# Performance work log

Hardware: AMD Instinct MI355X
Metric: run time of the kernel (lower is better)

## Reference

```python
import jax, jax.numpy as jnp
import numpy as np

D_MODEL, D_K, D_V, H = 1024, 128, 128, 8


def setup_inputs() -> dict:
    key = jax.random.key(0)
    ks = jax.random.split(key, 14)
    B, NQ, NK = 8, 1024, 1024
    def lin(kw, out_d, in_d):
        # xavier_uniform weight, zero bias
        lim = jnp.sqrt(6.0 / (in_d + out_d))
        return jax.random.uniform(kw, (out_d, in_d), jnp.float32, -lim, lim)
    return {
        "queries": jax.random.normal(ks[0], (B, NQ, D_MODEL), jnp.float32),
        "keys": jax.random.normal(ks[1], (B, NK, D_MODEL), jnp.float32),
        "values": jax.random.normal(ks[2], (B, NK, D_MODEL), jnp.float32),
        "language_signals": jax.random.normal(ks[3], (B, NQ, D_MODEL), jnp.float32),
        "Wq": lin(ks[4], H * D_K, D_MODEL), "bq": jnp.zeros((H * D_K,), jnp.float32),
        "Wk": lin(ks[5], H * D_K, D_MODEL), "bk": jnp.zeros((H * D_K,), jnp.float32),
        "Wv": lin(ks[6], H * D_V, D_MODEL), "bv": jnp.zeros((H * D_V,), jnp.float32),
        "Ws": lin(ks[7], H * D_K, D_MODEL), "bs": jnp.zeros((H * D_K,), jnp.float32),
        "Wo": lin(ks[8], D_MODEL, H * D_V), "bo": jnp.zeros((D_MODEL,), jnp.float32),
    }


def reference(queries, keys, values, language_signals,
              Wq, bq, Wk, bk, Wv, bv, Ws, bs, Wo, bo):
    b, nq, _ = queries.shape
    nk = keys.shape[1]
    scale = 1.0 / jnp.sqrt(jnp.asarray(D_K, queries.dtype))
    # project and split heads -> (b, h, n, d)
    q = (queries @ Wq.T + bq).reshape(b, nq, H, D_K).transpose(0, 2, 1, 3)
    s = (language_signals @ Ws.T + bs).reshape(b, nq, H, D_K).transpose(0, 2, 1, 3)
    k = (keys @ Wk.T + bk).reshape(b, nk, H, D_K).transpose(0, 2, 1, 3)
    v = (values @ Wv.T + bv).reshape(b, nk, H, D_V).transpose(0, 2, 1, 3)
    attn = jnp.einsum('bhqd,bhkd->bhqk', q, k) * scale           # (b,h,nq,nk)
    lang = jnp.einsum('bhqd,bhqd->bhq', q, s) * scale            # diagonal sentinel score
    combined = jnp.concatenate([attn, lang[..., None]], axis=-1)  # (b,h,nq,nk+1)
    p = jax.nn.softmax(combined, axis=-1)
    # per-query value set is [v; s_i]: split matmul into kv part + sentinel part
    out = jnp.einsum('bhqk,bhkd->bhqd', p[..., :nk], v) + p[..., nk:] * s
    out = out.transpose(0, 2, 1, 3).reshape(b, nq, H * D_V)
    return out @ Wo.T + bo
```

## Files before the change

### kernel.cpp

```cpp
#include <hip/hip_runtime.h>
#include <hip/hip_bf16.h>


typedef __attribute__((ext_vector_type(8))) short s16x8;
typedef __attribute__((ext_vector_type(4))) float f32x4;
typedef __attribute__((ext_vector_type(16))) float f32x16;
typedef __attribute__((ext_vector_type(4))) unsigned int u32x4;

#define DEVI static __device__ __forceinline__

constexpr int BATCH = 8;
constexpr int SEQ   = 1024;
constexpr int NH    = 8;
constexpr int DH    = 128;
constexpr int DM    = 1024;

DEVI short bf16r(float f) {
  __hip_bfloat16 h = __float2bfloat16(f);
  return *reinterpret_cast<short*>(&h);
}
DEVI float bf2f(short s) {
  __hip_bfloat16 h;
  *reinterpret_cast<short*>(&h) = s;
  return __bfloat162float(h);
}
DEVI s16x8 cvt8(const float4& a, const float4& b) {
  s16x8 r;
  r[0] = bf16r(a.x); r[1] = bf16r(a.y); r[2] = bf16r(a.z); r[3] = bf16r(a.w);
  r[4] = bf16r(b.x); r[5] = bf16r(b.y); r[6] = bf16r(b.z); r[7] = bf16r(b.w);
  return r;
}
DEVI unsigned int pack2bf(float a, float b) {
  return (unsigned int)(unsigned short)bf16r(a) |
         ((unsigned int)(unsigned short)bf16r(b) << 16);
}

#define GLOAD16(g, l)                                                        \
  __builtin_amdgcn_global_load_lds(                                          \
      (const __attribute__((address_space(1))) unsigned int*)(g),            \
      (__attribute__((address_space(3))) unsigned int*)(l), 16, 0, 0)

DEVI f32x4 mfma(s16x8 a, s16x8 b, f32x4 c) {
  return __builtin_amdgcn_mfma_f32_16x16x32_bf16(a, b, c, 0, 0, 0);
}
DEVI f32x16 mfma32(s16x8 a, s16x8 b, f32x16 c) {
  return __builtin_amdgcn_mfma_f32_32x32x16_bf16(a, b, c, 0, 0, 0);
}

__global__ __launch_bounds__(256)
void cvt_all(const float* __restrict__ a0, const float* __restrict__ a1,
             const float* __restrict__ a2, const float* __restrict__ a3,
             const float* __restrict__ w0, const float* __restrict__ w1,
             const float* __restrict__ w2, const float* __restrict__ w3,
             const float* __restrict__ w4,
             short* __restrict__ d0, short* __restrict__ d1,
             short* __restrict__ d2, short* __restrict__ d3,
             short* __restrict__ e0, short* __restrict__ e1,
             short* __restrict__ e2, short* __restrict__ e3,
             short* __restrict__ e4) {
  const float* s; short* d; int idx;
  int bid = blockIdx.x;
  if (bid < 16384) {
    int which = bid >> 12; idx = bid & 4095;
    switch (which) {
      case 0: s = a0; d = d0; break;
      case 1: s = a1; d = d1; break;
      case 2: s = a2; d = d2; break;
      default: s = a3; d = d3; break;
    }
  } else {
    int r = bid - 16384;
    int which = r >> 9; idx = r & 511;
    switch (which) {
      case 0: s = w0; d = e0; break;
      case 1: s = w1; d = e1; break;
      case 2: s = w2; d = e2; break;
      case 3: s = w3; d = e3; break;
      default: s = w4; d = e4; break;
    }
  }
  size_t i = ((size_t)idx * 256 + threadIdx.x) * 8;
  float4 a = *(const float4*)(s + i);
  float4 b = *(const float4*)(s + i + 4);
  *(s16x8*)(d + i) = cvt8(a, b);
}

DEVI void gemm_core(const short* __restrict__ A, const short* __restrict__ W,
                    short* Alds, short* Blds, int m0, int n0,
                    f32x4 (&acc)[4][4]) {
  const int tid = threadIdx.x, lane = tid & 63, wid = tid >> 6;
  const int wm = wid >> 1, wn = wid & 1, lr = lane & 15, lg = lane >> 4;
  const int srow = wid * 32 + (lane >> 3);
  const int scb  = (lane & 7) * 16;

  for (int k0 = 0; k0 < DM; k0 += 64) {
    if (k0) __syncthreads();
#pragma unroll
    for (int t = 0; t < 4; t++) {
      int row = srow + t * 8;
      int cbs = scb ^ ((row & 7) << 4);
      GLOAD16((const char*)A + ((size_t)(m0 + row) * DM + k0) * 2 + cbs,
              (char*)Alds + wid * 4096 + t * 1024);
      GLOAD16((const char*)W + ((size_t)(n0 + row) * DM + k0) * 2 + cbs,
              (char*)Blds + wid * 4096 + t * 1024);
    }
    __syncthreads();
#pragma unroll
    for (int kk = 0; kk < 2; kk++) {
      s16x8 af[4], bf[4];
#pragma unroll
      for (int i = 0; i < 4; i++) {
        int row = wm * 64 + i * 16 + lr;
        af[i] = *(const s16x8*)((const char*)Alds + row * 128 +
                                ((kk * 64 + lg * 16) ^ ((row & 7) << 4)));
      }
#pragma unroll
      for (int j = 0; j < 4; j++) {
        int row = wn * 64 + j * 16 + lr;
        bf[j] = *(const s16x8*)((const char*)Blds + row * 128 +
                                ((kk * 64 + lg * 16) ^ ((row & 7) << 4)));
      }
#pragma unroll
      for (int i = 0; i < 4; i++)
#pragma unroll
        for (int j = 0; j < 4; j++)
          acc[i][j] = mfma(af[i], bf[j], acc[i][j]);
    }
  }
}

__global__ __launch_bounds__(512, 2)
void proj_gemm256(const short* __restrict__ qa, const short* __restrict__ ka,
                  const short* __restrict__ va, const short* __restrict__ sa,
                  const short* __restrict__ wq, const short* __restrict__ wk,
                  const short* __restrict__ wv, const short* __restrict__ wsn,
                  const float* __restrict__ bq, const float* __restrict__ bk,
                  const float* __restrict__ bv, const float* __restrict__ bsn,
                  short* __restrict__ Qo, short* __restrict__ Ko,
                  short* __restrict__ Vo, short* __restrict__ So) {
  __shared__ short Alds[2][256 * 64];
  __shared__ short Blds[2][256 * 64];

  const int tid = threadIdx.x, lane = tid & 63, wid = tid >> 6;
  const int wm = wid >> 2, wn = wid & 3, lr = lane & 15, lg = lane >> 4;

  const int xcd = blockIdx.x & 7;
  const int r   = blockIdx.x >> 3;
  const int z   = xcd >> 1;
  const int m0  = (((xcd & 1) << 4) + (r >> 2)) << 8;
  const int n0  = (r & 3) << 8;

  const short* A; const short* W; const float* bias; short* C;
  switch (z) {
    case 0: A = qa; W = wq;  bias = bq;  C = Qo; break;
    case 1: A = ka; W = wk;  bias = bk;  C = Ko; break;
    case 2: A = va; W = wv;  bias = bv;  C = Vo; break;
    default: A = sa; W = wsn; bias = bsn; C = So; break;
  }
  const char* Ag = (const char*)A + (size_t)m0 * 2048;
  const char* Wg = (const char*)W + (size_t)n0 * 2048;

  const int sR  = wid * 8 + (lane >> 3);
  const int sCB = (((lane & 7) ^ (lane >> 3)) << 4);
  const int lgb = lg * 16, rsw = (lr & 7) << 4;
  const int ko0 = lgb ^ rsw, ko1 = (64 + lgb) ^ rsw;

#define STG(Gb, r0, kb, Lb, off)                                             \
  GLOAD16((Gb) + (size_t)((r0) + sR) * 2048 + (kb) + sCB,                    \
          (char*)(Lb) + (off) + wid * 1024)

  {
    char* pa0 = (char*)Alds[0]; char* pb0 = (char*)Blds[0];
    char* pa1 = (char*)Alds[1]; char* pb1 = (char*)Blds[1];
    STG(Ag,   0, 0, pa0, 0);     STG(Ag, 128, 0, pa0, 16384);
    STG(Ag,  64, 0, pa0, 8192);  STG(Ag, 192, 0, pa0, 24576);
    STG(Wg,   0, 0, pb0, 0);     STG(Wg,  64, 0, pb0, 8192);
    STG(Wg, 128, 0, pb0, 16384); STG(Wg, 192, 0, pb0, 24576);
    STG(Ag,   0, 128, pa1, 0);     STG(Ag, 128, 128, pa1, 16384);
    STG(Wg,   0, 128, pb1, 0);     STG(Wg,  64, 128, pb1, 8192);
    STG(Ag,  64, 128, pa1, 8192);  STG(Ag, 192, 128, pa1, 24576);
  }
  asm volatile("s_waitcnt vmcnt(6)" ::: "memory");
  __builtin_amdgcn_s_barrier();

  f32x4 acc[8][4] = {};
  const int rA0 = wm * 128 + lr;
  const int rB0 = wn * 64 + lr;

#pragma unroll 2
  for (int kt = 0; kt < 16; ++kt) {
    const char* Ab = (const char*)Alds[kt & 1];
    const char* Bb = (const char*)Blds[kt & 1];
    char* AbS = (char*)Alds[kt & 1];
    char* BbS = (char*)Blds[kt & 1];
    char* BbN = (char*)Blds[(kt + 1) & 1];
    const int kb1 = (kt + 1) * 128, kb2 = (kt + 2) * 128;

    s16x8 af[8], b0f[4], b1f[4];
#pragma unroll
    for (int mf = 0; mf < 4; mf++) {
      int ro = (rA0 + mf * 16) * 128;
      af[2 * mf]     = *(const s16x8*)(Ab + ro + ko0);
      af[2 * mf + 1] = *(const s16x8*)(Ab + ro + ko1);
    }
#pragma unroll
    for (int nf = 0; nf < 2; nf++) {
      int ro = (rB0 + nf * 16) * 128;
      b0f[2 * nf]     = *(const s16x8*)(Bb + ro + ko0);
      b0f[2 * nf + 1] = *(const s16x8*)(Bb + ro + ko1);
    }
    if (kt + 1 < 16) {
      STG(Wg, 128, kb1, BbN, 16384);
      STG(Wg, 192, kb1, BbN, 24576);
    }
    asm volatile("s_waitcnt lgkmcnt(8)" ::: "memory");
    __builtin_amdgcn_s_barrier();
    asm volatile("s_waitcnt lgkmcnt(0)" ::: "memory");
    __builtin_amdgcn_s_setprio(1);
#pragma unroll
    for (int mf = 0; mf < 4; mf++)
#pragma unroll
      for (int nf = 0; nf < 2; nf++) {
        acc[mf][nf] = mfma(af[2 * mf],     b0f[2 * nf],     acc[mf][nf]);
        acc[mf][nf] = mfma(af[2 * mf + 1], b0f[2 * nf + 1], acc[mf][nf]);
      }
    __builtin_amdgcn_s_setprio(0);
    __builtin_amdgcn_s_barrier();

#pragma unroll
    for (int nf = 0; nf < 2; nf++) {
      int ro = (rB0 + 32 + nf * 16) * 128;
      b1f[2 * nf]     = *(const s16x8*)(Bb + ro + ko0);
      b1f[2 * nf + 1] = *(const s16x8*)(Bb + ro + ko1);
    }
    if (kt + 2 < 16) {
      STG(Ag,   0, kb2, AbS, 0);
      STG(Ag, 128, kb2, AbS, 16384);
    }
    __builtin_amdgcn_s_barrier();
    asm volatile("s_waitcnt lgkmcnt(0)" ::: "memory");
    __builtin_amdgcn_s_setprio(1);
#pragma unroll
    for (int mf = 0; mf < 4; mf++)
#pragma unroll
      for (int nf = 0; nf < 2; nf++) {
        acc[mf][nf + 2] = mfma(af[2 * mf],     b1f[2 * nf],     acc[mf][nf + 2]);
        acc[mf][nf + 2] = mfma(af[2 * mf + 1], b1f[2 * nf + 1], acc[mf][nf + 2]);
      }
    __builtin_amdgcn_s_setprio(0);
    __builtin_amdgcn_s_barrier();

#pragma unroll
    for (int mf = 0; mf < 4; mf++) {
      int ro = (rA0 + 64 + mf * 16) * 128;
      af[2 * mf]     = *(const s16x8*)(Ab + ro + ko0);
      af[2 * mf + 1] = *(const s16x8*)(Ab + ro + ko1);
    }
    if (kt + 2 < 16) {
      STG(Wg,  0, kb2, BbS, 0);
      STG(Wg, 64, kb2, BbS, 8192);
    }
    __builtin_amdgcn_s_barrier();
    asm volatile("s_waitcnt lgkmcnt(0)" ::: "memory");
    __builtin_amdgcn_s_setprio(1);
#pragma unroll
    for (int mf = 0; mf < 4; mf++)
#pragma unroll
      for (int nf = 0; nf < 2; nf++) {
        acc[mf + 4][nf + 2] = mfma(af[2 * mf],     b1f[2 * nf],     acc[mf + 4][nf + 2]);
        acc[mf + 4][nf + 2] = mfma(af[2 * mf + 1], b1f[2 * nf + 1], acc[mf + 4][nf + 2]);
      }
    __builtin_amdgcn_s_setprio(0);
    __builtin_amdgcn_s_barrier();

    if (kt + 2 < 16) {
      STG(Ag,  64, kb2, AbS, 8192);
      STG(Ag, 192, kb2, AbS, 24576);
    }
    __builtin_amdgcn_s_barrier();
    __builtin_amdgcn_s_setprio(1);
#pragma unroll
    for (int mf = 0; mf < 4; mf++)
#pragma unroll
      for (int nf = 0; nf < 2; nf++) {
        acc[mf + 4][nf] = mfma(af[2 * mf],     b0f[2 * nf],     acc[mf + 4][nf]);
        acc[mf + 4][nf] = mfma(af[2 * mf + 1], b0f[2 * nf + 1], acc[mf + 4][nf]);
      }
    __builtin_amdgcn_s_setprio(0);
    if (kt < 14) asm volatile("s_waitcnt vmcnt(6)" ::: "memory");
    else         asm volatile("s_waitcnt vmcnt(0)" ::: "memory");
    __builtin_amdgcn_s_barrier();
  }
#undef STG

#pragma unroll
  for (int mf = 0; mf < 8; mf++) {
#pragma unroll
    for (int r2 = 0; r2 < 4; r2++) {
      int m = m0 + wm * 128 + mf * 16 + lg * 4 + r2;
      int bb = m >> 10, sq = m & 1023;
#pragma unroll
      for (int nf = 0; nf < 4; nf++) {
        int n = n0 + wn * 64 + nf * 16 + lr;
        float v = acc[mf][nf][r2] + bias[n];
        int hh = n >> 7, d = n & 127;
        if (z == 2)
          C[((size_t)(bb * NH + hh) * DH + d) * SEQ + sq] = bf16r(v);
        else
          C[((size_t)(bb * NH + hh) * SEQ + sq) * DH + d] = bf16r(v);
      }
    }
  }
}

__global__ __launch_bounds__(256)
void out_gemm(const short* __restrict__ A, const short* __restrict__ W,
              const float* __restrict__ bias, float* __restrict__ C) {
  __shared__ short Alds[128 * 64];
  __shared__ short Blds[128 * 64];
  const int bid = blockIdx.x;
  const int wg = (bid & 7) * 64 + (bid >> 3);
  const int m0 = (wg >> 3) * 128, n0 = (wg & 7) * 128;
  f32x4 acc[4][4] = {};
  gemm_core(A, W, Alds, Blds, m0, n0, acc);

  const int lane = threadIdx.x & 63, wid = threadIdx.x >> 6;
  const int wm = wid >> 1, wn = wid & 1, lr = lane & 15, lg = lane >> 4;
#pragma unroll
  for (int i = 0; i < 4; i++)
#pragma unroll
    for (int r = 0; r < 4; r++) {
      int m = m0 + wm * 64 + i * 16 + lg * 4 + r;
#pragma unroll
      for (int j = 0; j < 4; j++) {
        int n = n0 + wn * 64 + j * 16 + lr;
        C[(size_t)m * DM + n] = acc[i][j][r] + bias[n];
      }
    }
}

DEVI void stage_kv(const char* Kg, const char* Vg, int k0n,
                   short* Kd, short* Vd, int tid, int wave) {
  const int krow_l = tid >> 4, kslot = tid & 15;
  const int vrow_l = tid >> 3, vslot = tid & 7;
#pragma unroll
  for (int ln = 0; ln < 2; ln++) {
    int kr = ln * 32 + krow_l;
    int ss = kslot ^ (((kr & 7) << 1) ^ ((kr >> 3) & 3));
    GLOAD16(Kg + (size_t)(k0n + kr) * 256 + ss * 16,
            (char*)Kd + ln * 8192 + wave * 1024);
  }
#pragma unroll
  for (int ln = 0; ln < 2; ln++) {
    int dr = ln * 64 + vrow_l;
    int ss = vslot ^ ((dr & 7) ^ ((dr >> 3) & 3));
    GLOAD16(Vg + (size_t)dr * 2048 + (size_t)k0n * 2 + ss * 16,
            (char*)Vd + ln * 8192 + wave * 1024);
  }
}

__global__ __launch_bounds__(512, 2)
void attn_kernel(const short* __restrict__ Qb, const short* __restrict__ Kb,
                 const short* __restrict__ Vtb, const short* __restrict__ Sb,
                 short* __restrict__ att) {
  __shared__ short Klds[2][64 * 128];
  __shared__ short Vtlds[2][128 * 64];

  const int tid = threadIdx.x, lane = tid & 63, wave = tid >> 6;
  const int l31 = lane & 31, hi = lane >> 5;
  const int bid = blockIdx.x;
  const int logical = (bid & 7) * 32 + (bid >> 3);
  const int hb = logical >> 2, qt = logical & 3;
  const int b = hb >> 3, h = hb & 7;
  const int q0 = qt * 256 + wave * 32;
  const size_t base = (size_t)(b * NH + h) * SEQ * DH;
  const char* Kg = (const char*)(Kb + base);
  const char* Vg = (const char*)(Vtb + base);
  const float scale = 0.08838834764831845f * 1.44269504088896340f;

  s16x8 qf[8];
  {
    const char* qrow = (const char*)(Qb + base) + (size_t)(q0 + l31) * 256 + hi * 16;
#pragma unroll
    for (int kd = 0; kd < 8; kd++) qf[kd] = *(const s16x8*)(qrow + kd * 32);
  }

  float m_run = -INFINITY, l_run = 0.f;
  f32x16 oacc[4] = {};

  const int v4r = ((((lane & 7) << 1) ^ ((lane >> 3) & 3))) << 4;
  const int v3r = (((lane & 7) ^ ((lane >> 3) & 3))) << 4;

  stage_kv(Kg, Vg, 0, Klds[0], Vtlds[0], tid, wave);

  for (int it = 0; it < 16; ++it) {
    const int cur = it & 1;
    __syncthreads();
    if (it < 15)
      stage_kv(Kg, Vg, (it + 1) * 64, Klds[cur ^ 1], Vtlds[cur ^ 1], tid, wave);

    f32x16 st0 = {}, st1 = {};
    const char* Kb0 = (const char*)Klds[cur] + l31 * 256;
    __builtin_amdgcn_s_setprio(1);
#pragma unroll
    for (int kd = 0; kd < 8; kd++) {
      int co = (kd * 32 + hi * 16) ^ v4r;
      s16x8 a0 = *(const s16x8*)(Kb0 + co);
      s16x8 a1 = *(const s16x8*)(Kb0 + 32 * 256 + co);
      st0 = mfma32(a0, qf[kd], st0);
      st1 = mfma32(a1, qf[kd], st1);
    }
    __builtin_amdgcn_s_setprio(0);

    float traw = -INFINITY;
#pragma unroll
    for (int r = 0; r < 16; r++) {
      traw = fmaxf(traw, st0[r]);
      traw = fmaxf(traw, st1[r]);
    }
    traw = fmaxf(traw, __shfl_xor(traw, 32));
    float tmax = traw * scale;
    const bool skip = __all(tmax - m_run <= 8.f);
    float m_new = skip ? m_run : fmaxf(m_run, tmax);
    float psum = 0.f;
    unsigned W0[8], W1[8];
#pragma unroll
    for (int i = 0; i < 8; i++) {
      float p0 = exp2f(fmaf(st0[2 * i],     scale, -m_new));
      float p1 = exp2f(fmaf(st0[2 * i + 1], scale, -m_new));
      float p2 = exp2f(fmaf(st1[2 * i],     scale, -m_new));
      float p3 = exp2f(fmaf(st1[2 * i + 1], scale, -m_new));
      psum += (p0 + p1) + (p2 + p3);
      W0[i] = pack2bf(p0, p1);
      W1[i] = pack2bf(p2, p3);
    }
    psum += __shfl_xor(psum, 32);
    if (skip) {
      l_run += psum;
    } else {
      float fac = exp2f(m_run - m_new);
      l_run = l_run * fac + psum;
      m_run = m_new;
#pragma unroll
      for (int reg = 0; reg < 16; reg++) {
        int qs = (reg & 3) + 8 * (reg >> 2);
        float fr = __shfl(fac, qs + 4 * hi);
#pragma unroll
        for (int dt = 0; dt < 4; dt++) oacc[dt][reg] *= fr;
      }
    }

    s16x8 pa[4];
#pragma unroll
    for (int ks = 0; ks < 4; ks++) {
      const int s4 = (ks & 1) * 4;
      unsigned a0, a1, b0, b1;
      if (ks >> 1) { a0 = W1[s4]; a1 = W1[s4 + 1]; b0 = W1[s4 + 2]; b1 = W1[s4 + 3]; }
      else         { a0 = W0[s4]; a1 = W0[s4 + 1]; b0 = W0[s4 + 2]; b1 = W0[s4 + 3]; }
      unsigned snd0 = hi ? a0 : b0, snd1 = hi ? a1 : b1;
      unsigned rem0 = __shfl_xor(snd0, 32), rem1 = __shfl_xor(snd1, 32);
      unsigned w0 = hi ? rem0 : a0;
      unsigned w1 = hi ? rem1 : a1;
      unsigned w2 = hi ? b0 : rem0;
      unsigned w3 = hi ? b1 : rem1;
      u32x4 t4 = {w0, w1, w2, w3};
      pa[ks] = __builtin_bit_cast(s16x8, t4);
    }

    const char* Vb0 = (const char*)Vtlds[cur] + l31 * 128;
    __builtin_amdgcn_s_setprio(1);
#pragma unroll
    for (int dt = 0; dt < 4; dt++) {
#pragma unroll
      for (int ks = 0; ks < 4; ks++) {
        int co = (ks * 32 + hi * 16) ^ v3r;
        s16x8 bv = *(const s16x8*)(Vb0 + dt * 4096 + co);
        oacc[dt] = mfma32(pa[ks], bv, oacc[dt]);
      }
    }
    __builtin_amdgcn_s_setprio(0);
  }

  s16x8 sf[8];
  {
    const char* srow = (const char*)(Sb + base) + (size_t)(q0 + l31) * 256 + hi * 16;
#pragma unroll
    for (int kd = 0; kd < 8; kd++) sf[kd] = *(const s16x8*)(srow + kd * 32);
  }
  float dot = 0.f;
#pragma unroll
  for (int kd = 0; kd < 8; kd++)
#pragma unroll
    for (int j = 0; j < 8; j++) dot += bf2f(qf[kd][j]) * bf2f(sf[kd][j]);
  dot += __shfl_xor(dot, 32);
  float sc = dot * scale;
  float m_new = fmaxf(m_run, sc);
  float fac = exp2f(m_run - m_new);
  float ps = exp2f(sc - m_new);
  l_run = l_run * fac + ps;
  float inv_l = 1.f / l_run;

#pragma unroll
  for (int reg = 0; reg < 16; reg++) {
    int qs = (reg & 3) + 8 * (reg >> 2) + 4 * hi;
    int qsl = (reg & 3) + 8 * (reg >> 2);
    float fr = __shfl(fac,   qsl + 4 * hi);
    float pr = __shfl(ps,    qsl + 4 * hi);
    float il = __shfl(inv_l, qsl + 4 * hi);
    int qg = q0 + qs;
    const short* Sr = Sb + base + (size_t)qg * DH;
    short* orow = att + ((size_t)b * SEQ + qg) * (NH * DH) + h * DH;
#pragma unroll
    for (int dt = 0; dt < 4; dt++) {
      int d = dt * 32 + l31;
      float v = oacc[dt][reg] * fr + pr * bf2f(Sr[d]);
      orow[d] = bf16r(v * il);
    }
  }
}

extern "C" void kernel_launch(void* const* d_in, const int* in_sizes, int n_in,
                              void* d_out, int out_size, void* d_ws, size_t ws_size,
                              hipStream_t stream) {
  const float* queries = (const float*)d_in[0];
  const float* keys    = (const float*)d_in[1];
  const float* values  = (const float*)d_in[2];
  const float* lang    = (const float*)d_in[3];
  const float* Wq = (const float*)d_in[4];  const float* bq = (const float*)d_in[5];
  const float* Wk = (const float*)d_in[6];  const float* bk = (const float*)d_in[7];
  const float* Wv = (const float*)d_in[8];  const float* bv = (const float*)d_in[9];
  const float* Ws = (const float*)d_in[10]; const float* bs = (const float*)d_in[11];
  const float* Wo = (const float*)d_in[12]; const float* bo = (const float*)d_in[13];
  float* out = (float*)d_out;

  short* ws = (short*)d_ws;
  const size_t NE = (size_t)BATCH * SEQ * DM;
  const size_t WE = (size_t)DM * DM;
  short* qbf = ws;
  short* kbf = qbf + NE;
  short* vbf = kbf + NE;
  short* sbf = vbf + NE;
  short* Qb  = sbf + NE;
  short* Kb  = Qb  + NE;
  short* Vtb = Kb  + NE;
  short* Sb  = Vtb + NE;
  short* wqb = Sb  + NE;
  short* wkb = wqb + WE;
  short* wvb = wkb + WE;
  short* wsb = wvb + WE;
  short* wob = wsb + WE;
  short* att = qbf;

  hipLaunchKernelGGL(cvt_all, dim3(16384 + 2560), dim3(256), 0, stream,
                     queries, keys, values, lang, Wq, Wk, Wv, Ws, Wo,
                     qbf, kbf, vbf, sbf, wqb, wkb, wvb, wsb, wob);

  hipLaunchKernelGGL(proj_gemm256, dim3(512), dim3(512), 0, stream,
                     qbf, kbf, vbf, sbf, wqb, wkb, wvb, wsb,
                     bq, bk, bv, bs, Qb, Kb, Vtb, Sb);

  hipLaunchKernelGGL(attn_kernel, dim3(256), dim3(512), 0, stream,
                     Qb, Kb, Vtb, Sb, att);

  hipLaunchKernelGGL(out_gemm, dim3(512), dim3(256), 0, stream,
                     att, wob, bo, out);
}
```

Before: 232.4 us.

## Reschedule GEMM main loop: early LDS fragment loads, fewer barriers, split A regs

```diff
diff --git a/kernel.cpp b/kernel.cpp
--- a/kernel.cpp
+++ b/kernel.cpp
@@ -196,12 +196,17 @@
     char* BbN = (char*)Blds[(kt + 1) & 1];
     const int kb1 = (kt + 1) * 128, kb2 = (kt + 2) * 128;
 
-    s16x8 af[8], b0f[4], b1f[4];
+    s16x8 af0[8], af1[8], b0f[4], b1f[4];
+
+    if (kt + 1 < 16) {
+      STG(Wg, 128, kb1, BbN, 16384);
+      STG(Wg, 192, kb1, BbN, 24576);
+    }
 #pragma unroll
     for (int mf = 0; mf < 4; mf++) {
       int ro = (rA0 + mf * 16) * 128;
-      af[2 * mf]     = *(const s16x8*)(Ab + ro + ko0);
-      af[2 * mf + 1] = *(const s16x8*)(Ab + ro + ko1);
+      af0[2 * mf]     = *(const s16x8*)(Ab + ro + ko0);
+      af0[2 * mf + 1] = *(const s16x8*)(Ab + ro + ko1);
     }
 #pragma unroll
     for (int nf = 0; nf < 2; nf++) {
@@ -209,66 +214,61 @@
       b0f[2 * nf]     = *(const s16x8*)(Bb + ro + ko0);
       b0f[2 * nf + 1] = *(const s16x8*)(Bb + ro + ko1);
     }
-    if (kt + 1 < 16) {
-      STG(Wg, 128, kb1, BbN, 16384);
-      STG(Wg, 192, kb1, BbN, 24576);
-    }
-    asm volatile("s_waitcnt lgkmcnt(8)" ::: "memory");
-    __builtin_amdgcn_s_barrier();
-    asm volatile("s_waitcnt lgkmcnt(0)" ::: "memory");
-    __builtin_amdgcn_s_setprio(1);
-#pragma unroll
-    for (int mf = 0; mf < 4; mf++)
-#pragma unroll
-      for (int nf = 0; nf < 2; nf++) {
-        acc[mf][nf] = mfma(af[2 * mf],     b0f[2 * nf],     acc[mf][nf]);
-        acc[mf][nf] = mfma(af[2 * mf + 1], b0f[2 * nf + 1], acc[mf][nf]);
-      }
-    __builtin_amdgcn_s_setprio(0);
-    __builtin_amdgcn_s_barrier();
-
 #pragma unroll
     for (int nf = 0; nf < 2; nf++) {
       int ro = (rB0 + 32 + nf * 16) * 128;
       b1f[2 * nf]     = *(const s16x8*)(Bb + ro + ko0);
       b1f[2 * nf + 1] = *(const s16x8*)(Bb + ro + ko1);
     }
+    asm volatile("s_waitcnt lgkmcnt(4)" ::: "memory");
+    __builtin_amdgcn_sched_barrier(0);
+    __builtin_amdgcn_s_setprio(1);
+#pragma unroll
+    for (int mf = 0; mf < 4; mf++)
+#pragma unroll
+      for (int nf = 0; nf < 2; nf++) {
+        acc[mf][nf] = mfma(af0[2 * mf],     b0f[2 * nf],     acc[mf][nf]);
+        acc[mf][nf] = mfma(af0[2 * mf + 1], b0f[2 * nf + 1], acc[mf][nf]);
+      }
+    __builtin_amdgcn_s_setprio(0);
+    __builtin_amdgcn_s_barrier();
+
     if (kt + 2 < 16) {
       STG(Ag,   0, kb2, AbS, 0);
       STG(Ag, 128, kb2, AbS, 16384);
     }
-    __builtin_amdgcn_s_barrier();
-    asm volatile("s_waitcnt lgkmcnt(0)" ::: "memory");
+#pragma unroll
+    for (int mf = 0; mf < 4; mf++) {
+      int ro = (rA0 + 64 + mf * 16) * 128;
+      af1[2 * mf]     = *(const s16x8*)(Ab + ro + ko0);
+      af1[2 * mf + 1] = *(const s16x8*)(Ab + ro + ko1);
+    }
+    asm volatile("s_waitcnt lgkmcnt(8)" ::: "memory");
+    __builtin_amdgcn_sched_barrier(0);
     __builtin_amdgcn_s_setprio(1);
 #pragma unroll
     for (int mf = 0; mf < 4; mf++)
 #pragma unroll
       for (int nf = 0; nf < 2; nf++) {
-        acc[mf][nf + 2] = mfma(af[2 * mf],     b1f[2 * nf],     acc[mf][nf + 2]);
-        acc[mf][nf + 2] = mfma(af[2 * mf + 1], b1f[2 * nf + 1], acc[mf][nf + 2]);
+        acc[mf][nf + 2] = mfma(af0[2 * mf],     b1f[2 * nf],     acc[mf][nf + 2]);
+        acc[mf][nf + 2] = mfma(af0[2 * mf + 1], b1f[2 * nf + 1], acc[mf][nf + 2]);
       }
     __builtin_amdgcn_s_setprio(0);
     __builtin_amdgcn_s_barrier();
 
-#pragma unroll
-    for (int mf = 0; mf < 4; mf++) {
-      int ro = (rA0 + 64 + mf * 16) * 128;
-      af[2 * mf]     = *(const s16x8*)(Ab + ro + ko0);
-      af[2 * mf + 1] = *(const s16x8*)(Ab + ro + ko1);
-    }
     if (kt + 2 < 16) {
       STG(Wg,  0, kb2, BbS, 0);
       STG(Wg, 64, kb2, BbS, 8192);
     }
-    __builtin_amdgcn_s_barrier();
     asm volatile("s_waitcnt lgkmcnt(0)" ::: "memory");
+    __builtin_amdgcn_sched_barrier(0);
     __builtin_amdgcn_s_setprio(1);
 #pragma unroll
     for (int mf = 0; mf < 4; mf++)
 #pragma unroll
       for (int nf = 0; nf < 2; nf++) {
-        acc[mf + 4][nf + 2] = mfma(af[2 * mf],     b1f[2 * nf],     acc[mf + 4][nf + 2]);
-        acc[mf + 4][nf + 2] = mfma(af[2 * mf + 1], b1f[2 * nf + 1], acc[mf + 4][nf + 2]);
+        acc[mf + 4][nf + 2] = mfma(af1[2 * mf],     b1f[2 * nf],     acc[mf + 4][nf + 2]);
+        acc[mf + 4][nf + 2] = mfma(af1[2 * mf + 1], b1f[2 * nf + 1], acc[mf + 4][nf + 2]);
       }
     __builtin_amdgcn_s_setprio(0);
     __builtin_amdgcn_s_barrier();
@@ -277,14 +277,13 @@
       STG(Ag,  64, kb2, AbS, 8192);
       STG(Ag, 192, kb2, AbS, 24576);
     }
-    __builtin_amdgcn_s_barrier();
     __builtin_amdgcn_s_setprio(1);
 #pragma unroll
     for (int mf = 0; mf < 4; mf++)
 #pragma unroll
       for (int nf = 0; nf < 2; nf++) {
-        acc[mf + 4][nf] = mfma(af[2 * mf],     b0f[2 * nf],     acc[mf + 4][nf]);
-        acc[mf + 4][nf] = mfma(af[2 * mf + 1], b0f[2 * nf + 1], acc[mf + 4][nf]);
+        acc[mf + 4][nf] = mfma(af1[2 * mf],     b0f[2 * nf],     acc[mf + 4][nf]);
+        acc[mf + 4][nf] = mfma(af1[2 * mf + 1], b0f[2 * nf + 1], acc[mf + 4][nf]);
       }
     __builtin_amdgcn_s_setprio(0);
     if (kt < 14) asm volatile("s_waitcnt vmcnt(6)" ::: "memory");
```

After: 243.1 us. 4.6% more time.
